# Performance work log

Measured on AMD Instinct MI355X. Metric: run time of the kernel, lower is better.

## Reference

```python
import jax, jax.numpy as jnp
import numpy as np

B, N, K = 64, 128, 16      # sentences, nodes per sentence, max neighbors per node
IN, H, C = 300, 256, 5     # in_dim, h_dim, num_class
NEG = -1e9


def _linear(k, fan_in, fan_out):
    kw, kb = jax.random.split(k)
    w = jax.random.normal(kw, (fan_in, fan_out), jnp.float32) / np.sqrt(fan_in)
    b = jax.random.normal(kb, (fan_out,), jnp.float32) * 0.01
    return w, b


def setup_inputs() -> dict:
    key = jax.random.key(0)
    ks = jax.random.split(key, 12)
    x = jax.random.normal(ks[0], (B, N, 1 + K, IN), jnp.float32)
    nbr_counts = jax.random.randint(ks[1], (B, N), 1, K + 1).astype(jnp.int32)
    Wx_w, Wx_b = _linear(ks[2], IN, H)
    Wh_w, Wh_b = _linear(ks[3], H, H)
    Uh_w, Uh_b = _linear(ks[4], H, H)
    Wg_w, Wg_b = _linear(ks[5], H, H)
    Ug_w, Ug_b = _linear(ks[6], H, H)
    Wa_w, Wa_b = _linear(ks[7], H, H)   # Attention.Wh
    V_w, V_b = _linear(ks[8], H, H)     # Attention.V
    Wc_w, Wc_b = _linear(ks[9], H, C)   # classifier
    return dict(x=x, nbr_counts=nbr_counts,
                Wx_w=Wx_w, Wx_b=Wx_b, Wh_w=Wh_w, Wh_b=Wh_b,
                Uh_w=Uh_w, Uh_b=Uh_b, Wg_w=Wg_w, Wg_b=Wg_b,
                Ug_w=Ug_w, Ug_b=Ug_b, Wa_w=Wa_w, Wa_b=Wa_b,
                V_w=V_w, V_b=V_b, Wc_w=Wc_w, Wc_b=Wc_b)


def reference(x, nbr_counts, Wx_w, Wx_b, Wh_w, Wh_b, Uh_w, Uh_b,
              Wg_w, Wg_b, Ug_w, Ug_b, Wa_w, Wa_b, V_w, V_b, Wc_w, Wc_b):
    # mask[b,n,k] = True if neighbor k is real
    mask = jnp.arange(K)[None, None, :] < nbr_counts[:, :, None]          # [B,N,K]
    h = jnp.tanh(x @ Wx_w + Wx_b)                                         # [B,N,1+K,H]
    center = h[:, :, 0, :]                                                # [B,N,H]
    neigh = h[:, :, 1:, :]                                                # [B,N,K,H]
    # per-node gated attention over neighbors (softmax over neighbor axis, per feature)
    temp = jax.nn.sigmoid((center @ Wh_w + Wh_b)[:, :, None, :]
                          + (neigh @ Uh_w + Uh_b))                        # [B,N,K,H]
    a = jax.nn.softmax(jnp.where(mask[..., None], temp, NEG), axis=2)     # [B,N,K,H]
    con = jnp.sum(a * neigh, axis=2)                                      # [B,N,H]
    gate = jax.nn.sigmoid(center @ Wg_w + Wg_b + con @ Ug_w + Ug_b)       # [B,N,H]
    z = gate * center + (1.0 - gate) * con                                # [B,N,H]
    # sentence-level attention pooling over nodes (softmax over node axis)
    av = jax.nn.softmax(jax.nn.sigmoid(z @ Wa_w + Wa_b) @ V_w + V_b, axis=1)
    sent = jnp.sum(av * z, axis=1)                                        # [B,H]
    return jax.nn.log_softmax(sent @ Wc_w + Wc_b, axis=-1)                # [B,C]
```

## Files before the change

kernel.cpp:

```cpp
#include <hip/hip_runtime.h>
#include <hip/hip_bf16.h>
#include <math.h>

typedef __attribute__((ext_vector_type(8))) short short8;
typedef __attribute__((ext_vector_type(4))) float floatx4;
typedef __hip_bfloat16 bf16;

#define LDSP 40

__device__ __forceinline__ float sigmoidf_(float v) { return 1.f / (1.f + __expf(-v)); }

template<bool DUAL>
__device__ __forceinline__ void gemm_core(
    const bf16* A0p, const bf16* A1p, int lda,
    const bf16* B0, const bf16* B1, int ldb,
    int ksteps, floatx4 acc[2][2], bf16* As, bf16* Bs)
{
  const int tid  = threadIdx.x;
  const int lane = tid & 63;
  const int wave = tid >> 6;
  const int wm = wave >> 1, wn = wave & 1;
  const int srow = tid >> 2, sseg = tid & 3;
  const size_t m0 = (size_t)blockIdx.x * 64;
  const size_t n0 = (size_t)blockIdx.y * 64;
  const int half = DUAL ? (ksteps >> 1) : ksteps;
  const int fr = lane & 15, kb = lane >> 4;

  #pragma unroll
  for (int i = 0; i < 2; ++i)
    #pragma unroll
    for (int j = 0; j < 2; ++j) acc[i][j] = {0.f, 0.f, 0.f, 0.f};

  for (int kt = 0; kt < ksteps; ++kt) {
    const bool second = DUAL && (kt >= half);
    const bf16* Ap = second ? A1p : A0p;
    const bf16* Bp = second ? B1 : B0;
    const int kbase = (second ? (kt - half) : kt) * 32 + sseg * 8;

    *(short8*)&As[srow * LDSP + sseg * 8] =
        *(const short8*)(Ap + (m0 + srow) * (size_t)lda + kbase);
    *(short8*)&Bs[srow * LDSP + sseg * 8] =
        *(const short8*)(Bp + (n0 + srow) * (size_t)ldb + kbase);
    __syncthreads();

    short8 a0 = *(const short8*)&As[(wm * 32 + fr)      * LDSP + kb * 8];
    short8 a1 = *(const short8*)&As[(wm * 32 + 16 + fr) * LDSP + kb * 8];
    short8 b0 = *(const short8*)&Bs[(wn * 32 + fr)      * LDSP + kb * 8];
    short8 b1 = *(const short8*)&Bs[(wn * 32 + 16 + fr) * LDSP + kb * 8];
    acc[0][0] = __builtin_amdgcn_mfma_f32_16x16x32_bf16(a0, b0, acc[0][0], 0, 0, 0);
    acc[0][1] = __builtin_amdgcn_mfma_f32_16x16x32_bf16(a0, b1, acc[0][1], 0, 0, 0);
    acc[1][0] = __builtin_amdgcn_mfma_f32_16x16x32_bf16(a1, b0, acc[1][0], 0, 0, 0);
    acc[1][1] = __builtin_amdgcn_mfma_f32_16x16x32_bf16(a1, b1, acc[1][1], 0, 0, 0);
    __syncthreads();
  }
}

#define EPI_PREAMBLE \
  const int tid = threadIdx.x, lane = tid & 63, wave = tid >> 6; \
  const int wm = wave >> 1, wn = wave & 1; \
  const int m0 = blockIdx.x * 64, n0 = blockIdx.y * 64; \
  const int rq = lane >> 4, col = lane & 15; \
  (void)m0;

__global__ void k_transpose(const float* __restrict__ src, bf16* __restrict__ dst,
                            int rows, int cols, int dld) {
  int idx = blockIdx.x * 256 + threadIdx.x;
  if (idx >= cols * dld) return;
  int c = idx / dld, r = idx - c * dld;
  float v = (r < rows) ? src[(size_t)r * cols + c] : 0.f;
  dst[idx] = __float2bfloat16(v);
}

__global__ __launch_bounds__(256) void k_gemm1_wide(
    const float* __restrict__ x, const bf16* __restrict__ WxT,
    const float* __restrict__ bx, bf16* __restrict__ center, bf16* __restrict__ neigh) {
  __shared__ bf16 As[64 * LDSP], Bs[256 * LDSP];
  const int tid  = threadIdx.x;
  const int lane = tid & 63;
  const int wave = tid >> 6;
  const int wm = wave >> 1, wn = wave & 1;
  const int srow = tid >> 2, sseg = tid & 3;
  const size_t m0 = (size_t)blockIdx.x * 64;
  const int fr = lane & 15, kb = lane >> 4;

  floatx4 acc[4][2][2];
  #pragma unroll
  for (int nt = 0; nt < 4; ++nt)
    #pragma unroll
    for (int i = 0; i < 2; ++i)
      #pragma unroll
      for (int j = 0; j < 2; ++j) acc[nt][i][j] = {0.f, 0.f, 0.f, 0.f};

  for (int kt = 0; kt < 10; ++kt) {
    const int kbase = kt * 32 + sseg * 8;
    {
      const float* Af = x + (m0 + srow) * (size_t)300 + kbase;
      union { bf16 b[8]; short8 v; } u;
      if (kbase + 8 <= 300) {
        float4 f0 = *(const float4*)Af;
        float4 f1 = *(const float4*)(Af + 4);
        u.b[0] = __float2bfloat16(f0.x); u.b[1] = __float2bfloat16(f0.y);
        u.b[2] = __float2bfloat16(f0.z); u.b[3] = __float2bfloat16(f0.w);
        u.b[4] = __float2bfloat16(f1.x); u.b[5] = __float2bfloat16(f1.y);
        u.b[6] = __float2bfloat16(f1.z); u.b[7] = __float2bfloat16(f1.w);
      } else {
        #pragma unroll
        for (int j = 0; j < 8; ++j)
          u.b[j] = __float2bfloat16((kbase + j < 300) ? Af[j] : 0.f);
      }
      *(short8*)&As[srow * LDSP + sseg * 8] = u.v;
    }
    #pragma unroll
    for (int it = 0; it < 4; ++it) {
      const int brow = it * 64 + srow;
      *(short8*)&Bs[brow * LDSP + sseg * 8] =
          *(const short8*)(WxT + (size_t)brow * 320 + kbase);
    }
    __syncthreads();

    short8 a0 = *(const short8*)&As[(wm * 32 + fr)      * LDSP + kb * 8];
    short8 a1 = *(const short8*)&As[(wm * 32 + 16 + fr) * LDSP + kb * 8];
    #pragma unroll
    for (int nt = 0; nt < 4; ++nt) {
      short8 b0 = *(const short8*)&Bs[(nt * 64 + wn * 32 + fr)      * LDSP + kb * 8];
      short8 b1 = *(const short8*)&Bs[(nt * 64 + wn * 32 + 16 + fr) * LDSP + kb * 8];
      acc[nt][0][0] = __builtin_amdgcn_mfma_f32_16x16x32_bf16(a0, b0, acc[nt][0][0], 0, 0, 0);
      acc[nt][0][1] = __builtin_amdgcn_mfma_f32_16x16x32_bf16(a0, b1, acc[nt][0][1], 0, 0, 0);
      acc[nt][1][0] = __builtin_amdgcn_mfma_f32_16x16x32_bf16(a1, b0, acc[nt][1][0], 0, 0, 0);
      acc[nt][1][1] = __builtin_amdgcn_mfma_f32_16x16x32_bf16(a1, b1, acc[nt][1][1], 0, 0, 0);
    }
    __syncthreads();
  }

  const int rq = lane >> 4, col = lane & 15;
  #pragma unroll
  for (int nt = 0; nt < 4; ++nt)
    #pragma unroll
    for (int i = 0; i < 2; ++i)
      #pragma unroll
      for (int j = 0; j < 2; ++j) {
        int gc = nt * 64 + wn * 32 + j * 16 + col;
        float bias = bx[gc];
        #pragma unroll
        for (int r = 0; r < 4; ++r) {
          int gm = (int)m0 + wm * 32 + i * 16 + rq * 4 + r;
          float v = tanhf(acc[nt][i][j][r] + bias);
          int node = gm / 17, slot = gm - node * 17;
          bf16 bv = __float2bfloat16(v);
          if (slot == 0) center[(size_t)node * 256 + gc] = bv;
          else           neigh[((size_t)node * 16 + (slot - 1)) * 256 + gc] = bv;
        }
      }
}

template<int ACT>
__global__ __launch_bounds__(256) void k_gemm_simple(
    const bf16* __restrict__ A, const bf16* __restrict__ Bt,
    const float* __restrict__ bias, void* __restrict__ outp) {
  __shared__ bf16 As[64 * LDSP], Bs[64 * LDSP];
  floatx4 acc[2][2];
  gemm_core<false>(A, nullptr, 256, Bt, nullptr, 256, 8, acc, As, Bs);
  EPI_PREAMBLE
  #pragma unroll
  for (int i = 0; i < 2; ++i)
    #pragma unroll
    for (int j = 0; j < 2; ++j) {
      int gc = n0 + wn * 32 + j * 16 + col;
      float b = bias[gc];
      #pragma unroll
      for (int r = 0; r < 4; ++r) {
        int gm = m0 + wm * 32 + i * 16 + rq * 4 + r;
        float v = acc[i][j][r] + b;
        if (ACT == 1) ((bf16*)outp)[(size_t)gm * 256 + gc] = __float2bfloat16(sigmoidf_(v));
        else          ((float*)outp)[(size_t)gm * 256 + gc] = v;
      }
    }
}

__global__ __launch_bounds__(256) void k_gemm_attn(
    const bf16* __restrict__ neigh, const bf16* __restrict__ UhT,
    const float* __restrict__ bu, const float* __restrict__ Ct,
    const int* __restrict__ cnts, bf16* __restrict__ con) {
  __shared__ bf16 As[64 * LDSP], Bs[64 * LDSP];
  floatx4 acc[2][2];
  gemm_core<false>(neigh, nullptr, 256, UhT, nullptr, 256, 8, acc, As, Bs);
  EPI_PREAMBLE
  #pragma unroll
  for (int i = 0; i < 2; ++i) {
    const int node = blockIdx.x * 4 + wm * 2 + i;
    const int cnt = cnts[node];
    #pragma unroll
    for (int j = 0; j < 2; ++j) {
      const int gc = n0 + wn * 32 + j * 16 + col;
      const float add = bu[gc] + Ct[(size_t)node * 256 + gc];
      float t[4];
      float mx = -1e30f;
      #pragma unroll
      for (int r = 0; r < 4; ++r) {
        int k = rq * 4 + r;
        t[r] = sigmoidf_(acc[i][j][r] + add);
        if (k < cnt) mx = fmaxf(mx, t[r]);
      }
      mx = fmaxf(mx, __shfl_xor(mx, 16, 64));
      mx = fmaxf(mx, __shfl_xor(mx, 32, 64));
      float ps = 0.f, cs = 0.f;
      #pragma unroll
      for (int r = 0; r < 4; ++r) {
        int k = rq * 4 + r;
        float p = (k < cnt) ? __expf(t[r] - mx) : 0.f;
        ps += p;
        cs += p * __bfloat162float(neigh[((size_t)node * 16 + k) * 256 + gc]);
      }
      ps += __shfl_xor(ps, 16, 64); ps += __shfl_xor(ps, 32, 64);
      cs += __shfl_xor(cs, 16, 64); cs += __shfl_xor(cs, 32, 64);
      if (rq == 0) con[(size_t)node * 256 + gc] = __float2bfloat16(cs / ps);
    }
  }
}

__global__ __launch_bounds__(256) void k_gemm_gate(
    const bf16* __restrict__ center, const bf16* __restrict__ con,
    const bf16* __restrict__ WgT, const bf16* __restrict__ UgT,
    const float* __restrict__ bg, const float* __restrict__ bug,
    bf16* __restrict__ zb, float* __restrict__ zf) {
  __shared__ bf16 As[64 * LDSP], Bs[64 * LDSP];
  floatx4 acc[2][2];
  gemm_core<true>(center, con, 256, WgT, UgT, 256, 16, acc, As, Bs);
  EPI_PREAMBLE
  #pragma unroll
  for (int i = 0; i < 2; ++i)
    #pragma unroll
    for (int j = 0; j < 2; ++j) {
      int gc = n0 + wn * 32 + j * 16 + col;
      float b2 = bg[gc] + bug[gc];
      #pragma unroll
      for (int r = 0; r < 4; ++r) {
        int gm = m0 + wm * 32 + i * 16 + rq * 4 + r;
        float g  = sigmoidf_(acc[i][j][r] + b2);
        float cv = __bfloat162float(center[(size_t)gm * 256 + gc]);
        float ov = __bfloat162float(con[(size_t)gm * 256 + gc]);
        float zv = g * cv + (1.f - g) * ov;
        zb[(size_t)gm * 256 + gc] = __float2bfloat16(zv);
        zf[(size_t)gm * 256 + gc] = zv;
      }
    }
}

__global__ __launch_bounds__(256) void k_rowsoftmax(
    const float* __restrict__ L, const float* __restrict__ zf, float* __restrict__ sent) {
  const int b = blockIdx.x, c = threadIdx.x;
  float m = -1e30f, s = 0.f, acc = 0.f;
  for (int n = 0; n < 128; ++n) {
    size_t idx = ((size_t)b * 128 + n) * 256 + c;
    float v = L[idx];
    if (v > m) { float sc = __expf(m - v); s *= sc; acc *= sc; m = v; }
    float p = __expf(v - m);
    s += p;
    acc += p * zf[idx];
  }
  sent[b * 256 + c] = acc / s;
}

__global__ __launch_bounds__(64) void k_final(
    const float* __restrict__ sent, const float* __restrict__ Wc,
    const float* __restrict__ bc, float* __restrict__ out) {
  const int b = blockIdx.x, l = threadIdx.x;
  float part[5] = {0.f, 0.f, 0.f, 0.f, 0.f};
  #pragma unroll
  for (int u = 0; u < 4; ++u) {
    int c = l * 4 + u;
    float sv = sent[b * 256 + c];
    #pragma unroll
    for (int j = 0; j < 5; ++j) part[j] += sv * Wc[c * 5 + j];
  }
  #pragma unroll
  for (int j = 0; j < 5; ++j)
    for (int d = 1; d < 64; d <<= 1) part[j] += __shfl_xor(part[j], d, 64);
  if (l == 0) {
    float lg[5], mx = -1e30f;
    #pragma unroll
    for (int j = 0; j < 5; ++j) { lg[j] = part[j] + bc[j]; mx = fmaxf(mx, lg[j]); }
    float ss = 0.f;
    #pragma unroll
    for (int j = 0; j < 5; ++j) ss += __expf(lg[j] - mx);
    float lse = logf(ss) + mx;
    #pragma unroll
    for (int j = 0; j < 5; ++j) out[b * 5 + j] = lg[j] - lse;
  }
}

extern "C" void kernel_launch(void* const* d_in, const int* in_sizes, int n_in,
                              void* d_out, int out_size, void* d_ws, size_t ws_size,
                              hipStream_t stream) {
  const float* x    = (const float*)d_in[0];
  const int*   cnts = (const int*)d_in[1];
  const float* Wx_w = (const float*)d_in[2];  const float* Wx_b = (const float*)d_in[3];
  const float* Wh_w = (const float*)d_in[4];  const float* Wh_b = (const float*)d_in[5];
  const float* Uh_w = (const float*)d_in[6];  const float* Uh_b = (const float*)d_in[7];
  const float* Wg_w = (const float*)d_in[8];  const float* Wg_b = (const float*)d_in[9];
  const float* Ug_w = (const float*)d_in[10]; const float* Ug_b = (const float*)d_in[11];
  const float* Wa_w = (const float*)d_in[12]; const float* Wa_b = (const float*)d_in[13];
  const float* V_w  = (const float*)d_in[14]; const float* V_b  = (const float*)d_in[15];
  const float* Wc_w = (const float*)d_in[16]; const float* Wc_b = (const float*)d_in[17];
  float* out = (float*)d_out;
  (void)in_sizes; (void)n_in; (void)out_size;

  char* ws = (char*)d_ws;
  size_t off = 0;
  auto alloc = [&](size_t bytes) -> char* {
    char* p = ws + off; off += (bytes + 255) & ~(size_t)255; return p;
  };
  bf16* WxT    = (bf16*)alloc(256 * 320 * sizeof(bf16));
  bf16* WhT    = (bf16*)alloc(256 * 256 * sizeof(bf16));
  bf16* UhT    = (bf16*)alloc(256 * 256 * sizeof(bf16));
  bf16* WgT    = (bf16*)alloc(256 * 256 * sizeof(bf16));
  bf16* UgT    = (bf16*)alloc(256 * 256 * sizeof(bf16));
  bf16* WaT    = (bf16*)alloc(256 * 256 * sizeof(bf16));
  bf16* VT     = (bf16*)alloc(256 * 256 * sizeof(bf16));
  bf16* center = (bf16*)alloc((size_t)8192 * 256 * 2);
  bf16* neigh  = (bf16*)alloc((size_t)131072 * 256 * 2);
  float* Ct    = (float*)alloc((size_t)8192 * 256 * 4);
  bf16* con    = (bf16*)alloc((size_t)8192 * 256 * 2);
  bf16* zb     = (bf16*)alloc((size_t)8192 * 256 * 2);
  float* zf    = (float*)alloc((size_t)8192 * 256 * 4);
  bf16* S      = (bf16*)alloc((size_t)8192 * 256 * 2);
  float* sent  = (float*)alloc((size_t)64 * 256 * 4);
  float* L     = Ct;
  if (off > ws_size) return;

  k_transpose<<<dim3(320), 256, 0, stream>>>(Wx_w, WxT, 300, 256, 320);
  k_transpose<<<dim3(256), 256, 0, stream>>>(Wh_w, WhT, 256, 256, 256);
  k_transpose<<<dim3(256), 256, 0, stream>>>(Uh_w, UhT, 256, 256, 256);
  k_transpose<<<dim3(256), 256, 0, stream>>>(Wg_w, WgT, 256, 256, 256);
  k_transpose<<<dim3(256), 256, 0, stream>>>(Ug_w, UgT, 256, 256, 256);
  k_transpose<<<dim3(256), 256, 0, stream>>>(Wa_w, WaT, 256, 256, 256);
  k_transpose<<<dim3(256), 256, 0, stream>>>(V_w,  VT,  256, 256, 256);

  k_gemm1_wide<<<dim3(2176), 256, 0, stream>>>(x, WxT, Wx_b, center, neigh);
  k_gemm_simple<0><<<dim3(128, 4), 256, 0, stream>>>(center, WhT, Wh_b, Ct);
  k_gemm_attn<<<dim3(2048, 4), 256, 0, stream>>>(neigh, UhT, Uh_b, Ct, cnts, con);
  k_gemm_gate<<<dim3(128, 4), 256, 0, stream>>>(center, con, WgT, UgT, Wg_b, Ug_b, zb, zf);
  k_gemm_simple<1><<<dim3(128, 4), 256, 0, stream>>>(zb, WaT, Wa_b, S);
  k_gemm_simple<0><<<dim3(128, 4), 256, 0, stream>>>(S, VT, V_b, L);
  k_rowsoftmax<<<dim3(64), 256, 0, stream>>>(L, zf, sent);
  k_final<<<dim3(64), 64, 0, stream>>>(sent, Wc_w, Wc_b, out);
}
```

Measured before the change: 462.0 us.

## Move all GEMMs to 128x128 MFMA tiles and batch weight transposes

Replaces the 64x64 GEMM core with a 128x128 tile core in which each wave computes a 64x64 sub-block with 16 MFMAs per k-step. This raises operand reuse from LDS and cuts the barrier count per FLOP. The first GEMM loses its 64x256 wide tile, converts fp32 to bf16 by bit truncation instead of rounding, and uses an exp-based tanh. The seven weight transposes are merged into one launch. Small GEMMs now launch only 128 blocks, which may underfill the GPU, and the larger accumulator raises register pressure.

```diff
diff --git a/kernel.cpp b/kernel.cpp
--- a/kernel.cpp
+++ b/kernel.cpp
@@ -6,170 +6,202 @@
 typedef __attribute__((ext_vector_type(4))) float floatx4;
 typedef __hip_bfloat16 bf16;
 
-#define LDSP 40
+#define LDSQ 40
 
 __device__ __forceinline__ float sigmoidf_(float v) { return 1.f / (1.f + __expf(-v)); }
-
-template<bool DUAL>
-__device__ __forceinline__ void gemm_core(
-    const bf16* A0p, const bf16* A1p, int lda,
-    const bf16* B0, const bf16* B1, int ldb,
-    int ksteps, floatx4 acc[2][2], bf16* As, bf16* Bs)
+__device__ __forceinline__ float tanhf_(float v) {
+  float e = __expf(2.f * v);
+  return 1.f - 2.f / (e + 1.f);
+}
+
+template<int AMODE, bool DUAL>
+__device__ __forceinline__ void gemm128_core(
+    const void* A0p, const void* A1p, int lda, int kvalid,
+    const bf16* B0, const bf16* B1, int ldb, int ksteps,
+    floatx4 acc[4][4], bf16* As, bf16* Bs)
 {
-  const int tid  = threadIdx.x;
-  const int lane = tid & 63;
-  const int wave = tid >> 6;
+  const int tid = threadIdx.x, lane = tid & 63, wave = tid >> 6;
   const int wm = wave >> 1, wn = wave & 1;
-  const int srow = tid >> 2, sseg = tid & 3;
-  const size_t m0 = (size_t)blockIdx.x * 64;
-  const size_t n0 = (size_t)blockIdx.y * 64;
+  const int srow = tid >> 1, sc = (tid & 1) * 16;
+  const size_t m0 = (size_t)blockIdx.x * 128;
+  const size_t n0 = (size_t)blockIdx.y * 128;
   const int half = DUAL ? (ksteps >> 1) : ksteps;
   const int fr = lane & 15, kb = lane >> 4;
 
   #pragma unroll
-  for (int i = 0; i < 2; ++i)
-    #pragma unroll
-    for (int j = 0; j < 2; ++j) acc[i][j] = {0.f, 0.f, 0.f, 0.f};
+  for (int i = 0; i < 4; ++i)
+    #pragma unroll
+    for (int j = 0; j < 4; ++j) acc[i][j] = {0.f, 0.f, 0.f, 0.f};
 
   for (int kt = 0; kt < ksteps; ++kt) {
     const bool second = DUAL && (kt >= half);
-    const bf16* Ap = second ? A1p : A0p;
+    const void* Ap = second ? A1p : A0p;
     const bf16* Bp = second ? B1 : B0;
-    const int kbase = (second ? (kt - half) : kt) * 32 + sseg * 8;
-
-    *(short8*)&As[srow * LDSP + sseg * 8] =
-        *(const short8*)(Ap + (m0 + srow) * (size_t)lda + kbase);
-    *(short8*)&Bs[srow * LDSP + sseg * 8] =
-        *(const short8*)(Bp + (n0 + srow) * (size_t)ldb + kbase);
+    const int kbase = (second ? (kt - half) : kt) * 32 + sc;
+
+    if (AMODE == 1) {
+      const float* Af = (const float*)Ap + (m0 + srow) * (size_t)lda + kbase;
+      unsigned u[16];
+      if (kbase + 16 <= kvalid) {
+        float4 q0 = *(const float4*)(Af);
+        float4 q1 = *(const float4*)(Af + 4);
+        float4 q2 = *(const float4*)(Af + 8);
+        float4 q3 = *(const float4*)(Af + 12);
+        u[0]=__float_as_uint(q0.x); u[1]=__float_as_uint(q0.y); u[2]=__float_as_uint(q0.z); u[3]=__float_as_uint(q0.w);
+        u[4]=__float_as_uint(q1.x); u[5]=__float_as_uint(q1.y); u[6]=__float_as_uint(q1.z); u[7]=__float_as_uint(q1.w);
+        u[8]=__float_as_uint(q2.x); u[9]=__float_as_uint(q2.y); u[10]=__float_as_uint(q2.z); u[11]=__float_as_uint(q2.w);
+        u[12]=__float_as_uint(q3.x); u[13]=__float_as_uint(q3.y); u[14]=__float_as_uint(q3.z); u[15]=__float_as_uint(q3.w);
+      } else {
+        #pragma unroll
+        for (int e = 0; e < 16; ++e)
+          u[e] = (kbase + e < kvalid) ? __float_as_uint(Af[e]) : 0u;
+      }
+      uint4 p0, p1;
+      p0.x = (u[1] & 0xFFFF0000u) | (u[0] >> 16);
+      p0.y = (u[3] & 0xFFFF0000u) | (u[2] >> 16);
+      p0.z = (u[5] & 0xFFFF0000u) | (u[4] >> 16);
+      p0.w = (u[7] & 0xFFFF0000u) | (u[6] >> 16);
+      p1.x = (u[9] & 0xFFFF0000u) | (u[8] >> 16);
+      p1.y = (u[11] & 0xFFFF0000u) | (u[10] >> 16);
+      p1.z = (u[13] & 0xFFFF0000u) | (u[12] >> 16);
+      p1.w = (u[15] & 0xFFFF0000u) | (u[14] >> 16);
+      *(uint4*)&As[srow * LDSQ + sc]     = p0;
+      *(uint4*)&As[srow * LDSQ + sc + 8] = p1;
+    } else {
+      const bf16* Ab = (const bf16*)Ap + (m0 + srow) * (size_t)lda + kbase;
+      *(short8*)&As[srow * LDSQ + sc]     = *(const short8*)Ab;
+      *(short8*)&As[srow * LDSQ + sc + 8] = *(const short8*)(Ab + 8);
+    }
+    {
+      const bf16* Bb = Bp + (n0 + srow) * (size_t)ldb + kbase;
+      *(short8*)&Bs[srow * LDSQ + sc]     = *(const short8*)Bb;
+      *(short8*)&Bs[srow * LDSQ + sc + 8] = *(const short8*)(Bb + 8);
+    }
     __syncthreads();
 
-    short8 a0 = *(const short8*)&As[(wm * 32 + fr)      * LDSP + kb * 8];
-    short8 a1 = *(const short8*)&As[(wm * 32 + 16 + fr) * LDSP + kb * 8];
-    short8 b0 = *(const short8*)&Bs[(wn * 32 + fr)      * LDSP + kb * 8];
-    short8 b1 = *(const short8*)&Bs[(wn * 32 + 16 + fr) * LDSP + kb * 8];
-    acc[0][0] = __builtin_amdgcn_mfma_f32_16x16x32_bf16(a0, b0, acc[0][0], 0, 0, 0);
-    acc[0][1] = __builtin_amdgcn_mfma_f32_16x16x32_bf16(a0, b1, acc[0][1], 0, 0, 0);
-    acc[1][0] = __builtin_amdgcn_mfma_f32_16x16x32_bf16(a1, b0, acc[1][0], 0, 0, 0);
-    acc[1][1] = __builtin_amdgcn_mfma_f32_16x16x32_bf16(a1, b1, acc[1][1], 0, 0, 0);
+    short8 a[4], b[4];
+    #pragma unroll
+    for (int i = 0; i < 4; ++i)
+      a[i] = *(const short8*)&As[(wm * 64 + i * 16 + fr) * LDSQ + kb * 8];
+    #pragma unroll
+    for (int j = 0; j < 4; ++j)
+      b[j] = *(const short8*)&Bs[(wn * 64 + j * 16 + fr) * LDSQ + kb * 8];
+    #pragma unroll
+    for (int i = 0; i < 4; ++i)
+      #pragma unroll
+      for (int j = 0; j < 4; ++j)
+        acc[i][j] = __builtin_amdgcn_mfma_f32_16x16x32_bf16(a[i], b[j], acc[i][j], 0, 0, 0);
     __syncthreads();
   }
 }
 
-#define EPI_PREAMBLE \
+#define EPI128 \
   const int tid = threadIdx.x, lane = tid & 63, wave = tid >> 6; \
   const int wm = wave >> 1, wn = wave & 1; \
-  const int m0 = blockIdx.x * 64, n0 = blockIdx.y * 64; \
+  const int m0 = blockIdx.x * 128, n0 = blockIdx.y * 128; \
   const int rq = lane >> 4, col = lane & 15; \
   (void)m0;
 
-__global__ void k_transpose(const float* __restrict__ src, bf16* __restrict__ dst,
-                            int rows, int cols, int dld) {
+struct TransPack {
+  const float* src[7];
+  bf16* dst[7];
+  int rows[7];
+  int dld[7];
+};
+__global__ __launch_bounds__(256) void k_transpose_all(TransPack p) {
+  const int w = blockIdx.y;
+  const int dld = p.dld[w];
   int idx = blockIdx.x * 256 + threadIdx.x;
-  if (idx >= cols * dld) return;
+  if (idx >= 256 * dld) return;
   int c = idx / dld, r = idx - c * dld;
-  float v = (r < rows) ? src[(size_t)r * cols + c] : 0.f;
-  dst[idx] = __float2bfloat16(v);
-}
-
-__global__ __launch_bounds__(256) void k_gemm1_wide(
+  float v = (r < p.rows[w]) ? p.src[w][(size_t)r * 256 + c] : 0.f;
+  p.dst[w][idx] = __float2bfloat16(v);
+}
+
+__global__ __launch_bounds__(256) void k_gemm1_128(
     const float* __restrict__ x, const bf16* __restrict__ WxT,
     const float* __restrict__ bx, bf16* __restrict__ center, bf16* __restrict__ neigh) {
-  __shared__ bf16 As[64 * LDSP], Bs[256 * LDSP];
-  const int tid  = threadIdx.x;
-  const int lane = tid & 63;
-  const int wave = tid >> 6;
-  const int wm = wave >> 1, wn = wave & 1;
-  const int srow = tid >> 2, sseg = tid & 3;
-  const size_t m0 = (size_t)blockIdx.x * 64;
-  const int fr = lane & 15, kb = lane >> 4;
-
-  floatx4 acc[4][2][2];
-  #pragma unroll
-  for (int nt = 0; nt < 4; ++nt)
-    #pragma unroll
-    for (int i = 0; i < 2; ++i)
-      #pragma unroll
-      for (int j = 0; j < 2; ++j) acc[nt][i][j] = {0.f, 0.f, 0.f, 0.f};
-
-  for (int kt = 0; kt < 10; ++kt) {
-    const int kbase = kt * 32 + sseg * 8;
-    {
-      const float* Af = x + (m0 + srow) * (size_t)300 + kbase;
-      union { bf16 b[8]; short8 v; } u;
-      if (kbase + 8 <= 300) {
-        float4 f0 = *(const float4*)Af;
-        float4 f1 = *(const float4*)(Af + 4);
-        u.b[0] = __float2bfloat16(f0.x); u.b[1] = __float2bfloat16(f0.y);
-        u.b[2] = __float2bfloat16(f0.z); u.b[3] = __float2bfloat16(f0.w);
-        u.b[4] = __float2bfloat16(f1.x); u.b[5] = __float2bfloat16(f1.y);
-        u.b[6] = __float2bfloat16(f1.z); u.b[7] = __float2bfloat16(f1.w);
-      } else {
-        #pragma unroll
-        for (int j = 0; j < 8; ++j)
-          u.b[j] = __float2bfloat16((kbase + j < 300) ? Af[j] : 0.f);
-      }
-      *(short8*)&As[srow * LDSP + sseg * 8] = u.v;
-    }
-    #pragma unroll
-    for (int it = 0; it < 4; ++it) {
-      const int brow = it * 64 + srow;
-      *(short8*)&Bs[brow * LDSP + sseg * 8] =
-          *(const short8*)(WxT + (size_t)brow * 320 + kbase);
-    }
-    __syncthreads();
-
-    short8 a0 = *(const short8*)&As[(wm * 32 + fr)      * LDSP + kb * 8];
-    short8 a1 = *(const short8*)&As[(wm * 32 + 16 + fr) * LDSP + kb * 8];
-    #pragma unroll
-    for (int nt = 0; nt < 4; ++nt) {
-      short8 b0 = *(const short8*)&Bs[(nt * 64 + wn * 32 + fr)      * LDSP + kb * 8];
-      short8 b1 = *(const short8*)&Bs[(nt * 64 + wn * 32 + 16 + fr) * LDSP + kb * 8];
-      acc[nt][0][0] = __builtin_amdgcn_mfma_f32_16x16x32_bf16(a0, b0, acc[nt][0][0], 0, 0, 0);
-      acc[nt][0][1] = __builtin_amdgcn_mfma_f32_16x16x32_bf16(a0, b1, acc[nt][0][1], 0, 0, 0);
-      acc[nt][1][0] = __builtin_amdgcn_mfma_f32_16x16x32_bf16(a1, b0, acc[nt][1][0], 0, 0, 0);
-      acc[nt][1][1] = __builtin_amdgcn_mfma_f32_16x16x32_bf16(a1, b1, acc[nt][1][1], 0, 0, 0);
-    }
-    __syncthreads();
-  }
-
-  const int rq = lane >> 4, col = lane & 15;
-  #pragma unroll
-  for (int nt = 0; nt < 4; ++nt)
-    #pragma unroll
-    for (int i = 0; i < 2; ++i)
-      #pragma unroll
-      for (int j = 0; j < 2; ++j) {
-        int gc = nt * 64 + wn * 32 + j * 16 + col;
-        float bias = bx[gc];
-        #pragma unroll
-        for (int r = 0; r < 4; ++r) {
-          int gm = (int)m0 + wm * 32 + i * 16 + rq * 4 + r;
-          float v = tanhf(acc[nt][i][j][r] + bias);
-          int node = gm / 17, slot = gm - node * 17;
-          bf16 bv = __float2bfloat16(v);
-          if (slot == 0) center[(size_t)node * 256 + gc] = bv;
-          else           neigh[((size_t)node * 16 + (slot - 1)) * 256 + gc] = bv;
-        }
-      }
+  __shared__ bf16 As[128 * LDSQ], Bs[128 * LDSQ];
+  floatx4 acc[4][4];
+  gemm128_core<1, false>(x, nullptr, 300, 300, WxT, nullptr, 320, 10, acc, As, Bs);
+  EPI128
+  #pragma unroll
+  for (int i = 0; i < 4; ++i)
+    #pragma unroll
+    for (int j = 0; j < 4; ++j) {
+      int gc = n0 + wn * 64 + j * 16 + col;
+      float bias = bx[gc];
+      #pragma unroll
+      for (int r = 0; r < 4; ++r) {
+        int gm = m0 + wm * 64 + i * 16 + rq * 4 + r;
+        float v = tanhf_(acc[i][j][r] + bias);
+        int node = gm / 17, slot = gm - node * 17;
+        bf16 bv = __float2bfloat16(v);
+        if (slot == 0) center[(size_t)node * 256 + gc] = bv;
+        else           neigh[((size_t)node * 16 + (slot - 1)) * 256 + gc] = bv;
+      }
+    }
+}
+
+__global__ __launch_bounds__(256) void k_gemm_attn_128(
+    const bf16* __restrict__ neigh, const bf16* __restrict__ UhT,
+    const float* __restrict__ bu, const float* __restrict__ Ct,
+    const int* __restrict__ cnts, bf16* __restrict__ con) {
+  __shared__ bf16 As[128 * LDSQ], Bs[128 * LDSQ];
+  floatx4 acc[4][4];
+  gemm128_core<0, false>(neigh, nullptr, 256, 256, UhT, nullptr, 256, 8, acc, As, Bs);
+  EPI128
+  #pragma unroll
+  for (int i = 0; i < 4; ++i) {
+    const int rbase = m0 + wm * 64 + i * 16;
+    const int node = rbase >> 4;
+    const int cnt = cnts[node];
+    #pragma unroll
+    for (int j = 0; j < 4; ++j) {
+      const int gc = n0 + wn * 64 + j * 16 + col;
+      const float add = bu[gc] + Ct[(size_t)node * 256 + gc];
+      float t[4];
+      float mx = -1e30f;
+      #pragma unroll
+      for (int r = 0; r < 4; ++r) {
+        int k = rq * 4 + r;
+        t[r] = sigmoidf_(acc[i][j][r] + add);
+        if (k < cnt) mx = fmaxf(mx, t[r]);
+      }
+      mx = fmaxf(mx, __shfl_xor(mx, 16, 64));
+      mx = fmaxf(mx, __shfl_xor(mx, 32, 64));
+      float ps = 0.f, cs = 0.f;
+      #pragma unroll
+      for (int r = 0; r < 4; ++r) {
+        int k = rq * 4 + r;
+        float p = (k < cnt) ? __expf(t[r] - mx) : 0.f;
+        ps += p;
+        cs += p * __bfloat162float(neigh[((size_t)(rbase + k)) * 256 + gc]);
+      }
+      ps += __shfl_xor(ps, 16, 64); ps += __shfl_xor(ps, 32, 64);
+      cs += __shfl_xor(cs, 16, 64); cs += __shfl_xor(cs, 32, 64);
+      if (rq == 0) con[(size_t)node * 256 + gc] = __float2bfloat16(cs / ps);
+    }
+  }
 }
 
 template<int ACT>
-__global__ __launch_bounds__(256) void k_gemm_simple(
+__global__ __launch_bounds__(256) void k_gemm_s128(
     const bf16* __restrict__ A, const bf16* __restrict__ Bt,
     const float* __restrict__ bias, void* __restrict__ outp) {
-  __shared__ bf16 As[64 * LDSP], Bs[64 * LDSP];
-  floatx4 acc[2][2];
-  gemm_core<false>(A, nullptr, 256, Bt, nullptr, 256, 8, acc, As, Bs);
-  EPI_PREAMBLE
-  #pragma unroll
-  for (int i = 0; i < 2; ++i)
-    #pragma unroll
-    for (int j = 0; j < 2; ++j) {
-      int gc = n0 + wn * 32 + j * 16 + col;
+  __shared__ bf16 As[128 * LDSQ], Bs[128 * LDSQ];
+  floatx4 acc[4][4];
+  gemm128_core<0, false>(A, nullptr, 256, 256, Bt, nullptr, 256, 8, acc, As, Bs);
+  EPI128
+  #pragma unroll
+  for (int i = 0; i < 4; ++i)
+    #pragma unroll
+    for (int j = 0; j < 4; ++j) {
+      int gc = n0 + wn * 64 + j * 16 + col;
       float b = bias[gc];
       #pragma unroll
       for (int r = 0; r < 4; ++r) {
-        int gm = m0 + wm * 32 + i * 16 + rq * 4 + r;
+        int gm = m0 + wm * 64 + i * 16 + rq * 4 + r;
         float v = acc[i][j][r] + b;
         if (ACT == 1) ((bf16*)outp)[(size_t)gm * 256 + gc] = __float2bfloat16(sigmoidf_(v));
         else          ((float*)outp)[(size_t)gm * 256 + gc] = v;
@@ -177,65 +209,24 @@
     }
 }
 
-__global__ __launch_bounds__(256) void k_gemm_attn(
-    const bf16* __restrict__ neigh, const bf16* __restrict__ UhT,
-    const float* __restrict__ bu, const float* __restrict__ Ct,
-    const int* __restrict__ cnts, bf16* __restrict__ con) {
-  __shared__ bf16 As[64 * LDSP], Bs[64 * LDSP];
-  floatx4 acc[2][2];
-  gemm_core<false>(neigh, nullptr, 256, UhT, nullptr, 256, 8, acc, As, Bs);
-  EPI_PREAMBLE
-  #pragma unroll
-  for (int i = 0; i < 2; ++i) {
-    const int node = blockIdx.x * 4 + wm * 2 + i;
-    const int cnt = cnts[node];
-    #pragma unroll
-    for (int j = 0; j < 2; ++j) {
-      const int gc = n0 + wn * 32 + j * 16 + col;
-      const float add = bu[gc] + Ct[(size_t)node * 256 + gc];
-      float t[4];
-      float mx = -1e30f;
-      #pragma unroll
-      for (int r = 0; r < 4; ++r) {
-        int k = rq * 4 + r;
-        t[r] = sigmoidf_(acc[i][j][r] + add);
-        if (k < cnt) mx = fmaxf(mx, t[r]);
-      }
-      mx = fmaxf(mx, __shfl_xor(mx, 16, 64));
-      mx = fmaxf(mx, __shfl_xor(mx, 32, 64));
-      float ps = 0.f, cs = 0.f;
-      #pragma unroll
-      for (int r = 0; r < 4; ++r) {
-        int k = rq * 4 + r;
-        float p = (k < cnt) ? __expf(t[r] - mx) : 0.f;
-        ps += p;
-        cs += p * __bfloat162float(neigh[((size_t)node * 16 + k) * 256 + gc]);
-      }
-      ps += __shfl_xor(ps, 16, 64); ps += __shfl_xor(ps, 32, 64);
-      cs += __shfl_xor(cs, 16, 64); cs += __shfl_xor(cs, 32, 64);
-      if (rq == 0) con[(size_t)node * 256 + gc] = __float2bfloat16(cs / ps);
-    }
-  }
-}
-
-__global__ __launch_bounds__(256) void k_gemm_gate(
+__global__ __launch_bounds__(256) void k_gate128(
     const bf16* __restrict__ center, const bf16* __restrict__ con,
     const bf16* __restrict__ WgT, const bf16* __restrict__ UgT,
     const float* __restrict__ bg, const float* __restrict__ bug,
     bf16* __restrict__ zb, float* __restrict__ zf) {
-  __shared__ bf16 As[64 * LDSP], Bs[64 * LDSP];
-  floatx4 acc[2][2];
-  gemm_core<true>(center, con, 256, WgT, UgT, 256, 16, acc, As, Bs);
-  EPI_PREAMBLE
-  #pragma unroll
-  for (int i = 0; i < 2; ++i)
-    #pragma unroll
-    for (int j = 0; j < 2; ++j) {
-      int gc = n0 + wn * 32 + j * 16 + col;
+  __shared__ bf16 As[128 * LDSQ], Bs[128 * LDSQ];
+  floatx4 acc[4][4];
+  gemm128_core<0, true>(center, con, 256, 256, WgT, UgT, 256, 16, acc, As, Bs);
+  EPI128
+  #pragma unroll
+  for (int i = 0; i < 4; ++i)
+    #pragma unroll
+    for (int j = 0; j < 4; ++j) {
+      int gc = n0 + wn * 64 + j * 16 + col;
       float b2 = bg[gc] + bug[gc];
       #pragma unroll
       for (int r = 0; r < 4; ++r) {
-        int gm = m0 + wm * 32 + i * 16 + rq * 4 + r;
+        int gm = m0 + wm * 64 + i * 16 + rq * 4 + r;
         float g  = sigmoidf_(acc[i][j][r] + b2);
         float cv = __bfloat162float(center[(size_t)gm * 256 + gc]);
         float ov = __bfloat162float(con[(size_t)gm * 256 + gc]);
@@ -328,20 +319,22 @@
   float* L     = Ct;
   if (off > ws_size) return;
 
-  k_transpose<<<dim3(320), 256, 0, stream>>>(Wx_w, WxT, 300, 256, 320);
-  k_transpose<<<dim3(256), 256, 0, stream>>>(Wh_w, WhT, 256, 256, 256);
-  k_transpose<<<dim3(256), 256, 0, stream>>>(Uh_w, UhT, 256, 256, 256);
-  k_transpose<<<dim3(256), 256, 0, stream>>>(Wg_w, WgT, 256, 256, 256);
-  k_transpose<<<dim3(256), 256, 0, stream>>>(Ug_w, UgT, 256, 256, 256);
-  k_transpose<<<dim3(256), 256, 0, stream>>>(Wa_w, WaT, 256, 256, 256);
-  k_transpose<<<dim3(256), 256, 0, stream>>>(V_w,  VT,  256, 256, 256);
-
-  k_gemm1_wide<<<dim3(2176), 256, 0, stream>>>(x, WxT, Wx_b, center, neigh);
-  k_gemm_simple<0><<<dim3(128, 4), 256, 0, stream>>>(center, WhT, Wh_b, Ct);
-  k_gemm_attn<<<dim3(2048, 4), 256, 0, stream>>>(neigh, UhT, Uh_b, Ct, cnts, con);
-  k_gemm_gate<<<dim3(128, 4), 256, 0, stream>>>(center, con, WgT, UgT, Wg_b, Ug_b, zb, zf);
-  k_gemm_simple<1><<<dim3(128, 4), 256, 0, stream>>>(zb, WaT, Wa_b, S);
-  k_gemm_simple<0><<<dim3(128, 4), 256, 0, stream>>>(S, VT, V_b, L);
+  TransPack tp;
+  tp.src[0] = Wx_w; tp.dst[0] = WxT; tp.rows[0] = 300; tp.dld[0] = 320;
+  tp.src[1] = Wh_w; tp.dst[1] = WhT; tp.rows[1] = 256; tp.dld[1] = 256;
+  tp.src[2] = Uh_w; tp.dst[2] = UhT; tp.rows[2] = 256; tp.dld[2] = 256;
+  tp.src[3] = Wg_w; tp.dst[3] = WgT; tp.rows[3] = 256; tp.dld[3] = 256;
+  tp.src[4] = Ug_w; tp.dst[4] = UgT; tp.rows[4] = 256; tp.dld[4] = 256;
+  tp.src[5] = Wa_w; tp.dst[5] = WaT; tp.rows[5] = 256; tp.dld[5] = 256;
+  tp.src[6] = V_w;  tp.dst[6] = VT;  tp.rows[6] = 256; tp.dld[6] = 256;
+  k_transpose_all<<<dim3(320, 7), 256, 0, stream>>>(tp);
+
+  k_gemm1_128<<<dim3(1088, 2), 256, 0, stream>>>(x, WxT, Wx_b, center, neigh);
+  k_gemm_s128<0><<<dim3(64, 2), 256, 0, stream>>>(center, WhT, Wh_b, Ct);
+  k_gemm_attn_128<<<dim3(1024, 2), 256, 0, stream>>>(neigh, UhT, Uh_b, Ct, cnts, con);
+  k_gate128<<<dim3(64, 2), 256, 0, stream>>>(center, con, WgT, UgT, Wg_b, Ug_b, zb, zf);
+  k_gemm_s128<1><<<dim3(64, 2), 256, 0, stream>>>(zb, WaT, Wa_b, S);
+  k_gemm_s128<0><<<dim3(64, 2), 256, 0, stream>>>(S, VT, V_b, L);
   k_rowsoftmax<<<dim3(64), 256, 0, stream>>>(L, zf, sent);
   k_final<<<dim3(64), 64, 0, stream>>>(sent, Wc_w, Wc_b, out);
 }
```

Result: slower. 484.3 us (+4.8%).
